# Optimization experiments

Measured on AMD Instinct MI355X. Metric: run time of the kernel, lower is better.

## Reference

```python
import jax, jax.numpy as jnp
import numpy as np

N_NODES = 20000
N_EDGES = 480000
HIDDEN = 128
EDGE_FEAT = 128
BN_EPS = 1e-5


def setup_inputs() -> dict:
    key = jax.random.key(0)
    ks = jax.random.split(key, 6)
    z_dim = 2 * HIDDEN + EDGE_FEAT
    h = jax.random.normal(ks[0], (N_NODES, HIDDEN), dtype=jnp.float32)
    e = jax.random.normal(ks[1], (N_EDGES, EDGE_FEAT), dtype=jnp.float32)
    src = jax.random.randint(ks[2], (N_EDGES,), 0, N_NODES, dtype=jnp.int32)
    dst = jax.random.randint(ks[3], (N_EDGES,), 0, N_NODES, dtype=jnp.int32)
    W = jax.random.normal(ks[4], (z_dim, 2 * HIDDEN), dtype=jnp.float32) / np.sqrt(z_dim)
    b = jax.random.normal(ks[5], (2 * HIDDEN,), dtype=jnp.float32) * 0.01
    gamma = jnp.ones((2 * HIDDEN,), dtype=jnp.float32)
    beta = jnp.zeros((2 * HIDDEN,), dtype=jnp.float32)
    return {"h": h, "e": e, "src": src, "dst": dst, "W": W, "b": b,
            "gamma": gamma, "beta": beta}


def reference(h, e, src, dst, W, b, gamma, beta):
    # Gather endpoint features per edge: z = [h_src, h_dst, e]  -> [E, z_dim]
    z = jnp.concatenate([h[src], h[dst], e], axis=1)
    # Linear
    z = z @ W + b  # [E, 2*HIDDEN]
    # BatchNorm1d over the edge batch (training-mode stats, biased variance)
    mean = jnp.mean(z, axis=0)
    var = jnp.mean(jnp.square(z - mean), axis=0)
    z = (z - mean) * jax.lax.rsqrt(var + BN_EPS) * gamma + beta
    # Gated softplus message
    nbr_filter, nbr_core = jnp.split(z, 2, axis=1)
    msg = jax.nn.sigmoid(nbr_filter) * jax.nn.softplus(nbr_core)  # [E, HIDDEN]
    # Segment-sum reduce into destination nodes
    agg = jax.ops.segment_sum(msg, dst, num_segments=N_NODES)  # [N, HIDDEN]
    # Residual + softplus (dropout=0.0)
    return jax.nn.softplus(h + agg)
```

## Files before the change

### kernel.cpp

```cpp
#include <hip/hip_runtime.h>
#include <hip/hip_bf16.h>
#include <math.h>

#define N_NODES 20000
#define N_EDGES 480000
#define HIDDEN  128
#define ZDIM    384
#define NOUT    256
#define BN_EPS  1e-5f

#define KH      192
#define LDA2    200
#define LDZH    136
#define LDA     392
#define LDZ     264

using bf16x8 = __attribute__((ext_vector_type(8))) short;
using f32x4  = __attribute__((ext_vector_type(4))) float;
using s16x4  = __attribute__((ext_vector_type(4))) short;

struct f32x8 { float4 a, b; };

__device__ __forceinline__ unsigned short f2b(float f) {
    union { float f; unsigned u; } v; v.f = f;
    unsigned r = v.u + 0x7fffu + ((v.u >> 16) & 1u);
    return (unsigned short)(r >> 16);
}
__device__ __forceinline__ float bflo(unsigned u) {
    union { unsigned x; float f; } v; v.x = u << 16; return v.f;
}
__device__ __forceinline__ float bfhi(unsigned u) {
    union { unsigned x; float f; } v; v.x = u & 0xffff0000u; return v.f;
}
__device__ __forceinline__ float b2f(unsigned short s) {
    union { unsigned u; float f; } v; v.u = ((unsigned)s) << 16; return v.f;
}
__device__ __forceinline__ float sigmoid_(float x) {
    return 1.f / (1.f + __expf(-x));
}
__device__ __forceinline__ float softplus_(float x) {
    return fmaxf(x, 0.f) + __logf(1.f + __expf(-fabsf(x)));
}
__device__ __forceinline__ f32x8 ld8(const float* p) {
    f32x8 r; r.a = *(const float4*)p; r.b = *(const float4*)(p + 4); return r;
}
__device__ __forceinline__ bf16x8 cvt8(f32x8 v) {
    bf16x8 pk;
    pk[0] = (short)f2b(v.a.x); pk[1] = (short)f2b(v.a.y);
    pk[2] = (short)f2b(v.a.z); pk[3] = (short)f2b(v.a.w);
    pk[4] = (short)f2b(v.b.x); pk[5] = (short)f2b(v.b.y);
    pk[6] = (short)f2b(v.b.z); pk[7] = (short)f2b(v.b.w);
    return pk;
}

__global__ void convW(const float* __restrict__ W, short* __restrict__ wt) {
    int n = blockIdx.x;
    for (int k = threadIdx.x; k < ZDIM; k += 256)
        wt[n * ZDIM + k] = (short)f2b(W[(size_t)k * NOUT + n]);
}

__global__ void bn_finalize(const float* __restrict__ stats,
                            const float* __restrict__ gamma,
                            const float* __restrict__ beta,
                            float* __restrict__ scaleC,
                            float* __restrict__ shiftC) {
    int c = threadIdx.x;
    float s = 0.f, q = 0.f;
    for (int p = 0; p < 64; ++p) {
        s += stats[p * 512 + c];
        q += stats[p * 512 + 256 + c];
    }
    const float invE = 1.f / (float)N_EDGES;
    float m   = s * invE;
    float var = q * invE - m * m;
    float inv = rsqrtf(var + BN_EPS);
    float sc  = gamma[c] * inv;
    scaleC[c] = sc;
    shiftC[c] = beta[c] - m * sc;
}

__global__ void hist_dst(const int* __restrict__ dst, int* __restrict__ counts) {
    int i = blockIdx.x * 256 + threadIdx.x;
    if (i < N_EDGES) atomicAdd(&counts[dst[i]], 1);
}

__global__ void scan_nodes(const int* __restrict__ counts, int* __restrict__ offs,
                           int* __restrict__ cursor) {
    __shared__ int part[1024];
    int t = threadIdx.x;
    int base = t * 20;
    int local[20]; int s = 0;
    #pragma unroll
    for (int k = 0; k < 20; ++k) {
        int idx = base + k;
        int v = (idx < N_NODES) ? counts[idx] : 0;
        local[k] = s; s += v;
    }
    part[t] = s; __syncthreads();
    for (int d = 1; d < 1024; d <<= 1) {
        int v = (t >= d) ? part[t - d] : 0;
        __syncthreads();
        part[t] += v;
        __syncthreads();
    }
    int pre = (t > 0) ? part[t - 1] : 0;
    #pragma unroll
    for (int k = 0; k < 20; ++k) {
        int idx = base + k;
        if (idx < N_NODES) { int o = pre + local[k]; offs[idx] = o; cursor[idx] = o; }
    }
}

__global__ void build_perm(const int* __restrict__ dst, int* __restrict__ cursor,
                           int* __restrict__ perm) {
    int i = blockIdx.x * 256 + threadIdx.x;
    if (i < N_EDGES) { int p = atomicAdd(&cursor[dst[i]], 1); perm[p] = i; }
}

__global__ __launch_bounds__(256)
void edge_gemm_main(const float* __restrict__ h, const float* __restrict__ e,
                    const int* __restrict__ src, const int* __restrict__ dst,
                    const short* __restrict__ wt,
                    float* __restrict__ stats, short* __restrict__ zout) {
    const int tid  = threadIdx.x;
    const int bm   = blockIdx.x;
    const int rowBase = bm * 64;
    const int lane = tid & 63;
    const int brow = lane & 15;
    const int kgo  = (lane >> 4) * 8;
    const int wv   = tid >> 6;
    const int wcol = wv * 64;

    __shared__ __align__(16) short lds[64 * LDA2];

    const short* wB[4];
    #pragma unroll
    for (int n = 0; n < 4; ++n)
        wB[n] = wt + (size_t)(wcol + n * 16 + brow) * ZDIM + kgo;

    f32x4 acc[4][4] = {};

    #pragma unroll
    for (int half = 0; half < 2; ++half) {
        #pragma unroll
        for (int j = 0; j < 6; ++j) {
            int u   = tid + j * 256;
            int r   = u / 24;
            int f0  = (u - r * 24) * 8;
            int kabs = half * KH + f0;
            int row = rowBase + r;
            const float* p;
            if (kabs < 128)      p = h + (size_t)src[row] * HIDDEN + kabs;
            else if (kabs < 256) p = h + (size_t)dst[row] * HIDDEN + (kabs - 128);
            else                 p = e + (size_t)row * HIDDEN + (kabs - 256);
            *(bf16x8*)&lds[r * LDA2 + f0] = cvt8(ld8(p));
        }
        __syncthreads();

        const int kb = half * KH;
        bf16x8 aC[4], bC[4];
        #pragma unroll
        for (int m = 0; m < 4; ++m)
            aC[m] = *(const bf16x8*)&lds[(m * 16 + brow) * LDA2 + kgo];
        #pragma unroll
        for (int n = 0; n < 4; ++n) bC[n] = *(const bf16x8*)(wB[n] + kb);

        #pragma unroll
        for (int kk = 0; kk < 6; ++kk) {
            bf16x8 aN[4], bN[4];
            if (kk < 5) {
                #pragma unroll
                for (int n = 0; n < 4; ++n)
                    bN[n] = *(const bf16x8*)(wB[n] + kb + (kk + 1) * 32);
                #pragma unroll
                for (int m = 0; m < 4; ++m)
                    aN[m] = *(const bf16x8*)&lds[(m * 16 + brow) * LDA2 + (kk + 1) * 32 + kgo];
            }
            #pragma unroll
            for (int m = 0; m < 4; ++m)
                #pragma unroll
                for (int n = 0; n < 4; ++n)
                    acc[m][n] = __builtin_amdgcn_mfma_f32_16x16x32_bf16(
                                    aC[m], bC[n], acc[m][n], 0, 0, 0);
            if (kk < 5) {
                #pragma unroll
                for (int m = 0; m < 4; ++m) aC[m] = aN[m];
                #pragma unroll
                for (int n = 0; n < 4; ++n) bC[n] = bN[n];
            }
        }
        __syncthreads();
    }

    {
        float* base = stats + (size_t)(bm & 63) * 512;
        #pragma unroll
        for (int n = 0; n < 4; ++n) {
            float s = 0.f, q = 0.f;
            #pragma unroll
            for (int m = 0; m < 4; ++m)
                #pragma unroll
                for (int r = 0; r < 4; ++r) {
                    float v = acc[m][n][r];
                    s += v; q += v * v;
                }
            s += __shfl_xor(s, 16, 64); s += __shfl_xor(s, 32, 64);
            q += __shfl_xor(q, 16, 64); q += __shfl_xor(q, 32, 64);
            if (lane < 16) {
                int col = wcol + n * 16 + lane;
                atomicAdd(base + col, s);
                atomicAdd(base + 256 + col, q);
            }
        }
    }

    #pragma unroll
    for (int zh = 0; zh < 2; ++zh) {
        if ((wv >> 1) == zh) {
            #pragma unroll
            for (int m = 0; m < 4; ++m) {
                int rowb = m * 16 + (lane >> 4) * 4;
                #pragma unroll
                for (int n = 0; n < 4; ++n) {
                    int col = wcol + n * 16 + brow - zh * 128;
                    #pragma unroll
                    for (int r = 0; r < 4; ++r)
                        lds[(rowb + r) * LDZH + col] = (short)f2b(acc[m][n][r]);
                }
            }
        }
        __syncthreads();
        #pragma unroll
        for (int it = 0; it < 4; ++it) {
            int chunk = tid + it * 256;
            int r = chunk >> 4;
            int c = (chunk & 15) * 8;
            *(bf16x8*)&zout[((size_t)rowBase + r) * NOUT + zh * 128 + c] =
                *(const bf16x8*)&lds[r * LDZH + c];
        }
        __syncthreads();
    }
}

template<int MODE>
__global__ __launch_bounds__(256)
void edge_gemm_fb(const float* __restrict__ h, const float* __restrict__ e,
                  const int* __restrict__ src, const int* __restrict__ dst,
                  const short* __restrict__ wt,
                  float* __restrict__ stats,
                  const float* __restrict__ scaleC, const float* __restrict__ shiftC,
                  float* __restrict__ agg) {
    const int tid  = threadIdx.x;
    const int bm   = blockIdx.x;
    const int rowBase = bm * 64;
    const int lane = tid & 63;
    const int brow = lane & 15;
    const int kgo  = (lane >> 4) * 8;
    const int wcol = (tid >> 6) * 64;

    __shared__ __align__(16) short lds[64 * LDA];

    #pragma unroll
    for (int j = 0; j < 12; ++j) {
        int u = tid + j * 256;
        int r = u / 48;
        int f0 = (u - r * 48) * 8;
        int row = rowBase + r;
        const float* p;
        if (f0 < 128)      p = h + (size_t)src[row] * HIDDEN + f0;
        else if (f0 < 256) p = h + (size_t)dst[row] * HIDDEN + (f0 - 128);
        else               p = e + (size_t)row * HIDDEN + (f0 - 256);
        *(bf16x8*)&lds[r * LDA + f0] = cvt8(ld8(p));
    }
    __syncthreads();

    const short* wB[4];
    #pragma unroll
    for (int n = 0; n < 4; ++n)
        wB[n] = wt + (size_t)(wcol + n * 16 + brow) * ZDIM + kgo;

    f32x4 acc[4][4] = {};
    #pragma unroll
    for (int kk = 0; kk < 12; ++kk) {
        bf16x8 aC[4], bC[4];
        #pragma unroll
        for (int m = 0; m < 4; ++m)
            aC[m] = *(const bf16x8*)&lds[(m * 16 + brow) * LDA + kk * 32 + kgo];
        #pragma unroll
        for (int n = 0; n < 4; ++n) bC[n] = *(const bf16x8*)(wB[n] + kk * 32);
        #pragma unroll
        for (int m = 0; m < 4; ++m)
            #pragma unroll
            for (int n = 0; n < 4; ++n)
                acc[m][n] = __builtin_amdgcn_mfma_f32_16x16x32_bf16(
                                aC[m], bC[n], acc[m][n], 0, 0, 0);
    }

    if (MODE == 1) {
        float* base = stats + (size_t)(bm & 63) * 512;
        #pragma unroll
        for (int n = 0; n < 4; ++n) {
            float s = 0.f, q = 0.f;
            #pragma unroll
            for (int m = 0; m < 4; ++m)
                #pragma unroll
                for (int r = 0; r < 4; ++r) {
                    float v = acc[m][n][r]; s += v; q += v * v;
                }
            s += __shfl_xor(s, 16, 64); s += __shfl_xor(s, 32, 64);
            q += __shfl_xor(q, 16, 64); q += __shfl_xor(q, 32, 64);
            if (lane < 16) {
                int col = wcol + n * 16 + lane;
                atomicAdd(base + col, s);
                atomicAdd(base + 256 + col, q);
            }
        }
    } else {
        float sc[4], sh[4];
        #pragma unroll
        for (int n = 0; n < 4; ++n) {
            int col = wcol + n * 16 + brow;
            sc[n] = scaleC[col]; sh[n] = shiftC[col];
        }
        __syncthreads();
        #pragma unroll
        for (int m = 0; m < 4; ++m) {
            int rowb = m * 16 + (lane >> 4) * 4;
            #pragma unroll
            for (int n = 0; n < 4; ++n) {
                int col = wcol + n * 16 + brow;
                #pragma unroll
                for (int r = 0; r < 4; ++r)
                    lds[(rowb + r) * LDZ + col] = (short)f2b(acc[m][n][r] * sc[n] + sh[n]);
            }
        }
        __syncthreads();
        const int c0 = (tid & 31) * 4;
        const int r0 = tid >> 5;
        #pragma unroll
        for (int rp = 0; rp < 8; ++rp) {
            int row = rp * 8 + r0;
            int d   = dst[rowBase + row];
            float* ap = agg + (size_t)d * HIDDEN + c0;
            s16x4 f4 = *(const s16x4*)&lds[row * LDZ + c0];
            s16x4 c4 = *(const s16x4*)&lds[row * LDZ + 128 + c0];
            #pragma unroll
            for (int j = 0; j < 4; ++j)
                atomicAdd(ap + j, sigmoid_(b2f((unsigned short)f4[j])) *
                                  softplus_(b2f((unsigned short)c4[j])));
        }
    }
}

__global__ __launch_bounds__(256)
void node_gather(const short* __restrict__ z, const int* __restrict__ perm,
                 const int* __restrict__ offs, const int* __restrict__ counts,
                 const float* __restrict__ scaleC, const float* __restrict__ shiftC,
                 const float* __restrict__ h, float* __restrict__ out) {
    int node = blockIdx.x * 4 + (threadIdx.x >> 6);
    int lane = threadIdx.x & 63;
    int l32  = lane & 31;
    int c0   = l32 * 4;

    float scF[4], shF[4], scS[4], shS[4];
    #pragma unroll
    for (int k = 0; k < 4; ++k) {
        scF[k] = scaleC[c0 + k];       shF[k] = shiftC[c0 + k];
        scS[k] = scaleC[128 + c0 + k]; shS[k] = shiftC[128 + c0 + k];
    }

    int s   = offs[node];
    int deg = counts[node];
    float a0 = 0.f, a1 = 0.f, a2 = 0.f, a3 = 0.f;

    for (int j = (lane >> 5); j < deg; j += 4) {
        int jB = j + 2;
        bool hasB = (jB < deg);
        int eA = perm[s + j];
        int eB = hasB ? perm[s + jB] : eA;
        const short* zA = z + (size_t)eA * NOUT + c0;
        const short* zB = z + (size_t)eB * NOUT + c0;
        uint2 fA = *(const uint2*)zA;
        uint2 cA = *(const uint2*)(zA + 128);
        uint2 fB = *(const uint2*)zB;
        uint2 cB = *(const uint2*)(zB + 128);

        float f0 = bflo(fA.x) * scF[0] + shF[0];
        float f1 = bfhi(fA.x) * scF[1] + shF[1];
        float f2 = bflo(fA.y) * scF[2] + shF[2];
        float f3 = bfhi(fA.y) * scF[3] + shF[3];
        float g0 = bflo(cA.x) * scS[0] + shS[0];
        float g1 = bfhi(cA.x) * scS[1] + shS[1];
        float g2 = bflo(cA.y) * scS[2] + shS[2];
        float g3 = bfhi(cA.y) * scS[3] + shS[3];
        a0 += sigmoid_(f0) * softplus_(g0);
        a1 += sigmoid_(f1) * softplus_(g1);
        a2 += sigmoid_(f2) * softplus_(g2);
        a3 += sigmoid_(f3) * softplus_(g3);

        if (hasB) {
            f0 = bflo(fB.x) * scF[0] + shF[0];
            f1 = bfhi(fB.x) * scF[1] + shF[1];
            f2 = bflo(fB.y) * scF[2] + shF[2];
            f3 = bfhi(fB.y) * scF[3] + shF[3];
            g0 = bflo(cB.x) * scS[0] + shS[0];
            g1 = bfhi(cB.x) * scS[1] + shS[1];
            g2 = bflo(cB.y) * scS[2] + shS[2];
            g3 = bfhi(cB.y) * scS[3] + shS[3];
            a0 += sigmoid_(f0) * softplus_(g0);
            a1 += sigmoid_(f1) * softplus_(g1);
            a2 += sigmoid_(f2) * softplus_(g2);
            a3 += sigmoid_(f3) * softplus_(g3);
        }
    }
    a0 += __shfl_xor(a0, 32, 64);
    a1 += __shfl_xor(a1, 32, 64);
    a2 += __shfl_xor(a2, 32, 64);
    a3 += __shfl_xor(a3, 32, 64);

    if (lane < 32) {
        size_t o = (size_t)node * HIDDEN + c0;
        float4 hv = *(const float4*)&h[o];
        float4 r;
        r.x = softplus_(hv.x + a0);
        r.y = softplus_(hv.y + a1);
        r.z = softplus_(hv.z + a2);
        r.w = softplus_(hv.w + a3);
        *(float4*)&out[o] = r;
    }
}

__global__ void node_finalize(const float* __restrict__ h, float* __restrict__ out) {
    int i = blockIdx.x * 256 + threadIdx.x;
    float4 hv = ((const float4*)h)[i];
    float4 av = ((float4*)out)[i];
    float4 r;
    r.x = softplus_(hv.x + av.x);
    r.y = softplus_(hv.y + av.y);
    r.z = softplus_(hv.z + av.z);
    r.w = softplus_(hv.w + av.w);
    ((float4*)out)[i] = r;
}

extern "C" void kernel_launch(void* const* d_in, const int* in_sizes, int n_in,
                              void* d_out, int out_size, void* d_ws, size_t ws_size,
                              hipStream_t stream) {
    const float* h     = (const float*)d_in[0];
    const float* e     = (const float*)d_in[1];
    const int*   srcp  = (const int*)d_in[2];
    const int*   dstp  = (const int*)d_in[3];
    const float* W     = (const float*)d_in[4];
    const float* gamma = (const float*)d_in[6];
    const float* beta  = (const float*)d_in[7];
    float* out = (float*)d_out;

    char*  ws     = (char*)d_ws;
    float* stats  = (float*)ws;
    float* scaleC = (float*)(ws + 131072);
    float* shiftC = (float*)(ws + 132096);
    short* wt     = (short*)(ws + 133120);
    int*   counts = (int*)(ws + 329728);
    int*   offs   = (int*)(ws + 409856);
    int*   cursor = (int*)(ws + 489984);
    int*   perm   = (int*)(ws + 570112);
    short* zbuf   = (short*)(ws + 2490112);
    const size_t need = 2490112ull + (size_t)N_EDGES * NOUT * 2;

    hipMemsetAsync(stats, 0, 131072, stream);
    convW<<<NOUT, 256, 0, stream>>>(W, wt);

    if (ws_size >= need) {
        hipMemsetAsync(counts, 0, N_NODES * sizeof(int), stream);
        hist_dst<<<(N_EDGES + 255) / 256, 256, 0, stream>>>(dstp, counts);
        scan_nodes<<<1, 1024, 0, stream>>>(counts, offs, cursor);
        build_perm<<<(N_EDGES + 255) / 256, 256, 0, stream>>>(dstp, cursor, perm);

        edge_gemm_main<<<N_EDGES / 64, 256, 0, stream>>>(h, e, srcp, dstp, wt,
                stats, zbuf);
        bn_finalize<<<1, 256, 0, stream>>>(stats, gamma, beta, scaleC, shiftC);
        node_gather<<<N_NODES / 4, 256, 0, stream>>>(zbuf, perm, offs, counts,
                scaleC, shiftC, h, out);
    } else {
        hipMemsetAsync(out, 0, (size_t)N_NODES * HIDDEN * sizeof(float), stream);
        edge_gemm_fb<1><<<N_EDGES / 64, 256, 0, stream>>>(h, e, srcp, dstp, wt,
                stats, nullptr, nullptr, nullptr);
        bn_finalize<<<1, 256, 0, stream>>>(stats, gamma, beta, scaleC, shiftC);
        edge_gemm_fb<2><<<N_EDGES / 64, 256, 0, stream>>>(h, e, srcp, dstp, wt,
                stats, scaleC, shiftC, out);
        node_finalize<<<N_NODES * HIDDEN / (4 * 256), 256, 0, stream>>>(h, out);
    }
}
```

Before: 564.7 us.

## Scatter GEMM output into dst-sorted order and load A directly from global

The edge GEMM now drops the LDS staging of the gathered A tile and loads fp32 rows straight from global into registers, converting them to bf16 for 32x32x16 MFMAs. It writes each output row to its destination-sorted slot, using an inverse-position array built instead of a permutation. The node gather can then read z contiguously without the perm indirection. The cost is scattered 2-byte global stores from the GEMM, which may coalesce poorly, and A loads that are no longer shared through LDS.

```diff
diff --git a/kernel.cpp b/kernel.cpp
--- a/kernel.cpp
+++ b/kernel.cpp
@@ -9,14 +9,12 @@
 #define NOUT    256
 #define BN_EPS  1e-5f
 
-#define KH      192
-#define LDA2    200
-#define LDZH    136
 #define LDA     392
 #define LDZ     264
 
 using bf16x8 = __attribute__((ext_vector_type(8))) short;
 using f32x4  = __attribute__((ext_vector_type(4))) float;
+using f32x16 = __attribute__((ext_vector_type(16))) float;
 using s16x4  = __attribute__((ext_vector_type(4))) short;
 
 struct f32x8 { float4 a, b; };
@@ -111,103 +109,89 @@
     }
 }
 
-__global__ void build_perm(const int* __restrict__ dst, int* __restrict__ cursor,
-                           int* __restrict__ perm) {
+__global__ void build_ipos(const int* __restrict__ dst, int* __restrict__ cursor,
+                           int* __restrict__ ipos) {
     int i = blockIdx.x * 256 + threadIdx.x;
-    if (i < N_EDGES) { int p = atomicAdd(&cursor[dst[i]], 1); perm[p] = i; }
-}
-
-__global__ __launch_bounds__(256)
-void edge_gemm_main(const float* __restrict__ h, const float* __restrict__ e,
-                    const int* __restrict__ src, const int* __restrict__ dst,
-                    const short* __restrict__ wt,
-                    float* __restrict__ stats, short* __restrict__ zout) {
+    if (i < N_EDGES) ipos[i] = atomicAdd(&cursor[dst[i]], 1);
+}
+
+__global__ __launch_bounds__(256, 4)
+void edge_gemm_w(const float* __restrict__ h, const float* __restrict__ e,
+                 const int* __restrict__ src, const int* __restrict__ dst,
+                 const short* __restrict__ wt, const int* __restrict__ ipos,
+                 float* __restrict__ stats, short* __restrict__ zout) {
     const int tid  = threadIdx.x;
-    const int bm   = blockIdx.x;
-    const int rowBase = bm * 64;
     const int lane = tid & 63;
-    const int brow = lane & 15;
-    const int kgo  = (lane >> 4) * 8;
-    const int wv   = tid >> 6;
-    const int wcol = wv * 64;
-
-    __shared__ __align__(16) short lds[64 * LDA2];
-
-    const short* wB[4];
-    #pragma unroll
-    for (int n = 0; n < 4; ++n)
-        wB[n] = wt + (size_t)(wcol + n * 16 + brow) * ZDIM + kgo;
-
-    f32x4 acc[4][4] = {};
-
-    #pragma unroll
-    for (int half = 0; half < 2; ++half) {
-        #pragma unroll
-        for (int j = 0; j < 6; ++j) {
-            int u   = tid + j * 256;
-            int r   = u / 24;
-            int f0  = (u - r * 24) * 8;
-            int kabs = half * KH + f0;
-            int row = rowBase + r;
-            const float* p;
-            if (kabs < 128)      p = h + (size_t)src[row] * HIDDEN + kabs;
-            else if (kabs < 256) p = h + (size_t)dst[row] * HIDDEN + (kabs - 128);
-            else                 p = e + (size_t)row * HIDDEN + (kabs - 256);
-            *(bf16x8*)&lds[r * LDA2 + f0] = cvt8(ld8(p));
-        }
-        __syncthreads();
-
-        const int kb = half * KH;
-        bf16x8 aC[4], bC[4];
-        #pragma unroll
-        for (int m = 0; m < 4; ++m)
-            aC[m] = *(const bf16x8*)&lds[(m * 16 + brow) * LDA2 + kgo];
-        #pragma unroll
-        for (int n = 0; n < 4; ++n) bC[n] = *(const bf16x8*)(wB[n] + kb);
-
-        #pragma unroll
-        for (int kk = 0; kk < 6; ++kk) {
-            bf16x8 aN[4], bN[4];
-            if (kk < 5) {
+    const int l31  = lane & 31;
+    const int hi   = lane >> 5;
+    const int w    = tid >> 6;
+    const int rowBase = blockIdx.x * 64;
+    const int colBase = w * 64;
+
+    const float* pS[2]; const float* pD[2]; const float* pE[2];
+    #pragma unroll
+    for (int mi = 0; mi < 2; ++mi) {
+        int row = rowBase + mi * 32 + l31;
+        pS[mi] = h + (size_t)src[row] * HIDDEN + hi * 8;
+        pD[mi] = h + (size_t)dst[row] * HIDDEN + hi * 8;
+        pE[mi] = e + (size_t)row * HIDDEN + hi * 8;
+    }
+    const short* pB[2];
+    #pragma unroll
+    for (int n = 0; n < 2; ++n)
+        pB[n] = wt + (size_t)(colBase + n * 32 + l31) * ZDIM + hi * 8;
+
+    #define APTR(mi, kk) ((kk) < 8  ? pS[mi] + (kk) * 16 \
+                        : (kk) < 16 ? pD[mi] + ((kk) - 8) * 16 \
+                                    : pE[mi] + ((kk) - 16) * 16)
+
+    f32x16 acc[2][2] = {};
+    bf16x8 aC[2], bC[2];
+    #pragma unroll
+    for (int mi = 0; mi < 2; ++mi) aC[mi] = cvt8(ld8(APTR(mi, 0)));
+    #pragma unroll
+    for (int n = 0; n < 2; ++n) bC[n] = *(const bf16x8*)(pB[n]);
+
+    #pragma unroll
+    for (int kk = 0; kk < 24; ++kk) {
+        bf16x8 aN[2], bN[2];
+        if (kk < 23) {
+            #pragma unroll
+            for (int mi = 0; mi < 2; ++mi) aN[mi] = cvt8(ld8(APTR(mi, kk + 1)));
+            #pragma unroll
+            for (int n = 0; n < 2; ++n) bN[n] = *(const bf16x8*)(pB[n] + (kk + 1) * 16);
+        }
+        #pragma unroll
+        for (int mi = 0; mi < 2; ++mi)
+            #pragma unroll
+            for (int n = 0; n < 2; ++n)
+                acc[mi][n] = __builtin_amdgcn_mfma_f32_32x32x16_bf16(
+                                 aC[mi], bC[n], acc[mi][n], 0, 0, 0);
+        if (kk < 23) {
+            #pragma unroll
+            for (int mi = 0; mi < 2; ++mi) aC[mi] = aN[mi];
+            #pragma unroll
+            for (int n = 0; n < 2; ++n) bC[n] = bN[n];
+        }
+    }
+    #undef APTR
+
+    {
+        float* base = stats + (size_t)(blockIdx.x & 63) * 512;
+        #pragma unroll
+        for (int n = 0; n < 2; ++n) {
+            float s = 0.f, q = 0.f;
+            #pragma unroll
+            for (int mi = 0; mi < 2; ++mi)
                 #pragma unroll
-                for (int n = 0; n < 4; ++n)
-                    bN[n] = *(const bf16x8*)(wB[n] + kb + (kk + 1) * 32);
-                #pragma unroll
-                for (int m = 0; m < 4; ++m)
-                    aN[m] = *(const bf16x8*)&lds[(m * 16 + brow) * LDA2 + (kk + 1) * 32 + kgo];
-            }
-            #pragma unroll
-            for (int m = 0; m < 4; ++m)
-                #pragma unroll
-                for (int n = 0; n < 4; ++n)
-                    acc[m][n] = __builtin_amdgcn_mfma_f32_16x16x32_bf16(
-                                    aC[m], bC[n], acc[m][n], 0, 0, 0);
-            if (kk < 5) {
-                #pragma unroll
-                for (int m = 0; m < 4; ++m) aC[m] = aN[m];
-                #pragma unroll
-                for (int n = 0; n < 4; ++n) bC[n] = bN[n];
-            }
-        }
-        __syncthreads();
-    }
-
-    {
-        float* base = stats + (size_t)(bm & 63) * 512;
-        #pragma unroll
-        for (int n = 0; n < 4; ++n) {
-            float s = 0.f, q = 0.f;
-            #pragma unroll
-            for (int m = 0; m < 4; ++m)
-                #pragma unroll
-                for (int r = 0; r < 4; ++r) {
-                    float v = acc[m][n][r];
+                for (int r = 0; r < 16; ++r) {
+                    float v = acc[mi][n][r];
                     s += v; q += v * v;
                 }
-            s += __shfl_xor(s, 16, 64); s += __shfl_xor(s, 32, 64);
-            q += __shfl_xor(q, 16, 64); q += __shfl_xor(q, 32, 64);
-            if (lane < 16) {
-                int col = wcol + n * 16 + lane;
+            s += __shfl_xor(s, 32, 64);
+            q += __shfl_xor(q, 32, 64);
+            if (lane < 32) {
+                int col = colBase + n * 32 + l31;
                 atomicAdd(base + col, s);
                 atomicAdd(base + 256 + col, q);
             }
@@ -215,31 +199,16 @@
     }
 
     #pragma unroll
-    for (int zh = 0; zh < 2; ++zh) {
-        if ((wv >> 1) == zh) {
-            #pragma unroll
-            for (int m = 0; m < 4; ++m) {
-                int rowb = m * 16 + (lane >> 4) * 4;
-                #pragma unroll
-                for (int n = 0; n < 4; ++n) {
-                    int col = wcol + n * 16 + brow - zh * 128;
-                    #pragma unroll
-                    for (int r = 0; r < 4; ++r)
-                        lds[(rowb + r) * LDZH + col] = (short)f2b(acc[m][n][r]);
-                }
-            }
-        }
-        __syncthreads();
-        #pragma unroll
-        for (int it = 0; it < 4; ++it) {
-            int chunk = tid + it * 256;
-            int r = chunk >> 4;
-            int c = (chunk & 15) * 8;
-            *(bf16x8*)&zout[((size_t)rowBase + r) * NOUT + zh * 128 + c] =
-                *(const bf16x8*)&lds[r * LDZH + c];
-        }
-        __syncthreads();
-    }
+    for (int mi = 0; mi < 2; ++mi)
+        #pragma unroll
+        for (int r = 0; r < 16; ++r) {
+            int rowL = mi * 32 + 4 * hi + (r & 3) + 8 * (r >> 2);
+            int slot = ipos[rowBase + rowL];
+            #pragma unroll
+            for (int n = 0; n < 2; ++n)
+                zout[(size_t)slot * NOUT + colBase + n * 32 + l31] =
+                    (short)f2b(acc[mi][n][r]);
+        }
 }
 
 template<int MODE>
@@ -353,7 +322,7 @@
 }
 
 __global__ __launch_bounds__(256)
-void node_gather(const short* __restrict__ z, const int* __restrict__ perm,
+void node_gather(const short* __restrict__ z,
                  const int* __restrict__ offs, const int* __restrict__ counts,
                  const float* __restrict__ scaleC, const float* __restrict__ shiftC,
                  const float* __restrict__ h, float* __restrict__ out) {
@@ -376,10 +345,8 @@
     for (int j = (lane >> 5); j < deg; j += 4) {
         int jB = j + 2;
         bool hasB = (jB < deg);
-        int eA = perm[s + j];
-        int eB = hasB ? perm[s + jB] : eA;
-        const short* zA = z + (size_t)eA * NOUT + c0;
-        const short* zB = z + (size_t)eB * NOUT + c0;
+        const short* zA = z + (size_t)(s + j) * NOUT + c0;
+        const short* zB = z + (size_t)(s + (hasB ? jB : j)) * NOUT + c0;
         uint2 fA = *(const uint2*)zA;
         uint2 cA = *(const uint2*)(zA + 128);
         uint2 fB = *(const uint2*)zB;
@@ -462,7 +429,7 @@
     int*   counts = (int*)(ws + 329728);
     int*   offs   = (int*)(ws + 409856);
     int*   cursor = (int*)(ws + 489984);
-    int*   perm   = (int*)(ws + 570112);
+    int*   ipos   = (int*)(ws + 570112);
     short* zbuf   = (short*)(ws + 2490112);
     const size_t need = 2490112ull + (size_t)N_EDGES * NOUT * 2;
 
@@ -473,12 +440,12 @@
         hipMemsetAsync(counts, 0, N_NODES * sizeof(int), stream);
         hist_dst<<<(N_EDGES + 255) / 256, 256, 0, stream>>>(dstp, counts);
         scan_nodes<<<1, 1024, 0, stream>>>(counts, offs, cursor);
-        build_perm<<<(N_EDGES + 255) / 256, 256, 0, stream>>>(dstp, cursor, perm);
-
-        edge_gemm_main<<<N_EDGES / 64, 256, 0, stream>>>(h, e, srcp, dstp, wt,
+        build_ipos<<<(N_EDGES + 255) / 256, 256, 0, stream>>>(dstp, cursor, ipos);
+
+        edge_gemm_w<<<N_EDGES / 64, 256, 0, stream>>>(h, e, srcp, dstp, wt, ipos,
                 stats, zbuf);
         bn_finalize<<<1, 256, 0, stream>>>(stats, gamma, beta, scaleC, shiftC);
-        node_gather<<<N_NODES / 4, 256, 0, stream>>>(zbuf, perm, offs, counts,
+        node_gather<<<N_NODES / 4, 256, 0, stream>>>(zbuf, offs, counts,
                 scaleC, shiftC, h, out);
     } else {
         hipMemsetAsync(out, 0, (size_t)N_NODES * HIDDEN * sizeof(float), stream);
```

Result: slower. 780.9 us (+38.3%).
